# Optimization experiments

Hardware: AMD Instinct MI355X
Metric: run time of the kernel (lower is better)

The kernel has to match this reference:

```python
import jax, jax.numpy as jnp
import numpy as np

B, T_PREFIX, C_IN = 8, 6144, 8
OUT_LEN, OUT_C = 2048, 8
AUX_DIM = 16
D_MODEL, D_STATE, HEADDIM, EXPAND = 256, 32, 64, 2
D_INNER = EXPAND * D_MODEL            # 512
NHEADS = D_INNER // HEADDIM           # 8
CONV_DIM = D_INNER + 2 * D_STATE      # 576
D_PROJ = 2 * D_INNER + 2 * D_STATE + NHEADS  # 1096
N_LAYERS = 2
CHUNK = 64
PATCH = 16
PRECONV_K = 5
DCONV_K = 4


def setup_inputs() -> dict:
    key = jax.random.key(0)
    ks = iter(jax.random.split(key, 64))
    def rn(shape, s=0.02):
        return s * jax.random.normal(next(ks), shape, jnp.float32)
    inp = dict(
        x_prefix=jax.random.normal(next(ks), (B, T_PREFIX, C_IN), jnp.float32),
        y_aux=jax.random.normal(next(ks), (B, AUX_DIM), jnp.float32),
        pre_conv_w=rn((D_MODEL, C_IN, PRECONV_K), 0.1),
        pre_conv_b=rn((D_MODEL,)),
        patch_w=rn((D_MODEL, D_MODEL, PATCH), 0.05),
        patch_b=rn((D_MODEL,)),
        mask_token=rn((D_MODEL,)),
        aux_w=rn((AUX_DIM, D_MODEL), 0.1),
        aux_b=rn((D_MODEL,)),
        patch_out_w=rn((2 * D_MODEL, OUT_C * PATCH), 0.05),
        patch_out_b=rn((OUT_C * PATCH,)),
    )
    for d in ('fwd', 'bwd'):
        inp[f'{d}_norm_w'] = jnp.ones((N_LAYERS, D_MODEL), jnp.float32)
        inp[f'{d}_inproj'] = rn((N_LAYERS, D_MODEL, D_PROJ), 0.05)
        inp[f'{d}_conv_w'] = rn((N_LAYERS, CONV_DIM, DCONV_K), 0.2)
        inp[f'{d}_conv_b'] = rn((N_LAYERS, CONV_DIM))
        inp[f'{d}_dtbias'] = rn((N_LAYERS, NHEADS), 0.5)
        inp[f'{d}_Alog'] = jnp.tile(jnp.log(jnp.arange(1, NHEADS + 1, dtype=jnp.float32)), (N_LAYERS, 1))
        inp[f'{d}_D'] = jnp.ones((N_LAYERS, NHEADS), jnp.float32)
        inp[f'{d}_gnorm'] = jnp.ones((N_LAYERS, D_INNER), jnp.float32)
        inp[f'{d}_outproj'] = rn((N_LAYERS, D_INNER, D_MODEL), 0.05)
    return inp


def rmsnorm(x, w, eps=1e-5):
    return x * jax.lax.rsqrt(jnp.mean(x * x, axis=-1, keepdims=True) + eps) * w


def conv1d(x, w, b, stride, pad):  # x: [B,C,T], w: [O,I,K]
    y = jax.lax.conv_general_dilated(x, w, (stride,), [(pad, pad)],
                                     dimension_numbers=('NCH', 'OIH', 'NCH'))
    return y + b[None, :, None]


def mamba_block(u, inproj, conv_w, conv_b, dtbias, Alog, Dp, gnorm_w, outproj):
    # Mamba-2/SSD style block: in_proj -> z | xBC | dt, causal depthwise conv,
    # selective scan with per-head scalar decay A, +D skip, gated RMSNorm, out_proj.
    b, T, _ = u.shape
    zxbcdt = u @ inproj                                   # [b,T,D_PROJ]
    z = zxbcdt[..., :D_INNER]
    xBC = zxbcdt[..., D_INNER:D_INNER + CONV_DIM]
    dt = jax.nn.softplus(zxbcdt[..., -NHEADS:] + dtbias)  # [b,T,H]
    # causal depthwise conv over time
    xc = jax.lax.conv_general_dilated(xBC.transpose(0, 2, 1), conv_w[:, None, :], (1,),
                                      [(DCONV_K - 1, 0)],
                                      dimension_numbers=('NCH', 'OIH', 'NCH'),
                                      feature_group_count=CONV_DIM)
    xBC = jax.nn.silu((xc + conv_b[None, :, None]).transpose(0, 2, 1))
    xs = xBC[..., :D_INNER].reshape(b, T, NHEADS, HEADDIM)  # [b,T,H,P]
    Bm = xBC[..., D_INNER:D_INNER + D_STATE]                # [b,T,N]
    Cm = xBC[..., D_INNER + D_STATE:]                       # [b,T,N]
    A = -jnp.exp(Alog)                                      # [H]

    def step(h, inps):  # h: [b,H,P,N]
        dt_t, x_t, B_t, C_t = inps
        dA = jnp.exp(dt_t * A)[:, :, None, None]
        h = h * dA + (dt_t[:, :, None] * x_t)[..., None] * B_t[:, None, None, :]
        y = jnp.einsum('bhpn,bn->bhp', h, C_t)
        return h, y

    h0 = jnp.zeros((b, NHEADS, HEADDIM, D_STATE), u.dtype)
    _, ys = jax.lax.scan(step, h0, (dt.transpose(1, 0, 2), xs.transpose(1, 0, 2, 3),
                                    Bm.transpose(1, 0, 2), Cm.transpose(1, 0, 2)))
    y = ys.transpose(1, 0, 2, 3) + Dp[None, None, :, None] * xs
    y = y.reshape(b, T, D_INNER)
    y = rmsnorm(y * jax.nn.silu(z), gnorm_w)
    return y @ outproj


def reference(x_prefix, y_aux, pre_conv_w, pre_conv_b, patch_w, patch_b, mask_token,
              aux_w, aux_b, fwd_norm_w, fwd_inproj, fwd_conv_w, fwd_conv_b, fwd_dtbias,
              fwd_Alog, fwd_D, fwd_gnorm, fwd_outproj, bwd_norm_w, bwd_inproj,
              bwd_conv_w, bwd_conv_b, bwd_dtbias, bwd_Alog, bwd_D, bwd_gnorm,
              bwd_outproj, patch_out_w, patch_out_b):
    b = x_prefix.shape[0]
    t_total = T_PREFIX + OUT_LEN
    x_full = jnp.pad(x_prefix, ((0, 0), (0, OUT_LEN), (0, 0)))        # zeros for future
    x = jax.nn.silu(conv1d(x_full.transpose(0, 2, 1), pre_conv_w, pre_conv_b, 1, PRECONV_K // 2))
    x = conv1d(x, patch_w, patch_b, PATCH, 0).transpose(0, 2, 1)      # [b, n_tokens, d_model]
    n_tokens = x.shape[1]
    # eval mode: deterministic future-patch mask, dropout is identity
    starts = jnp.arange(n_tokens) * PATCH
    mask = (starts >= T_PREFIX)[None, :, None]
    x = jnp.where(mask, mask_token[None, None, :], x)
    aux_bias = jax.nn.silu(y_aux @ aux_w + aux_b)[:, None, :]
    x = x + aux_bias
    pad_t = (-n_tokens) % CHUNK
    if pad_t:
        x = jnp.pad(x, ((0, 0), (0, pad_t), (0, 0)))
    h_f = x
    h_b = x[:, ::-1]
    for i in range(N_LAYERS):
        h_f = h_f + mamba_block(rmsnorm(h_f, fwd_norm_w[i]), fwd_inproj[i], fwd_conv_w[i],
                                fwd_conv_b[i], fwd_dtbias[i], fwd_Alog[i], fwd_D[i],
                                fwd_gnorm[i], fwd_outproj[i])
        h_b = h_b + mamba_block(rmsnorm(h_b, bwd_norm_w[i]), bwd_inproj[i], bwd_conv_w[i],
                                bwd_conv_b[i], bwd_dtbias[i], bwd_Alog[i], bwd_D[i],
                                bwd_gnorm[i], bwd_outproj[i])
    h = jnp.concatenate([h_f, h_b[:, ::-1]], axis=-1)[:, :n_tokens]   # [b,n,2*d_model]
    patch_pred = h @ patch_out_w + patch_out_b                        # [b,n,out_c*patch]
    y = patch_pred.reshape(b, n_tokens, OUT_C, PATCH).reshape(b, n_tokens * PATCH, OUT_C)
    y = y[:, :t_total, :]
    return y[:, T_PREFIX:, :]
```

## Files before the change

kernel.cpp:

```cpp
#include <hip/hip_runtime.h>
#include <hip/hip_bf16.h>
#include <math.h>

#define BSZ      8
#define TPREF    6144
#define CIN      8
#define DMODEL   256
#define DINNER   512
#define DSTATE   32
#define NHEADS   8
#define HEADDIM  64
#define CONVDIM  576
#define DPROJ    1096
#define NTOK     512
#define NVIS     384
#define TBWD     128
#define MFWD     (BSZ * NTOK)
#define MBWD     (BSZ * TBWD)
#define MALL     (MFWD + MBWD)

typedef float f32x4 __attribute__((ext_vector_type(4)));
typedef __bf16 bf16x8 __attribute__((ext_vector_type(8)));

__device__ __forceinline__ float silu_f(float x) { return x / (1.f + expf(-x)); }

#define ASYNC16(gp, lp) \
    __builtin_amdgcn_global_load_lds((const __attribute__((address_space(1))) void*)(gp), \
                                     (__attribute__((address_space(3))) void*)(lp), 16, 0, 0)

__global__ __launch_bounds__(256) void gemm_mfma(
    const __bf16* __restrict__ A, const __bf16* __restrict__ Bt,
    float* __restrict__ C, const float* __restrict__ bias,
    int N, int K, int ldc, int flags, long pstr) {
    __shared__ char sm[16384];
    int tid = threadIdx.x;
    int m0 = blockIdx.y * 128, n0 = blockIdx.x * 128;
    int klen = K / gridDim.z;
    int kbeg = blockIdx.z * klen;
    int w = tid >> 6, l = tid & 63;
    int wm = w >> 1, wn = w & 1;
    int lm = l & 15, q = l >> 4;

    f32x4 acc[4][4];
    #pragma unroll
    for (int i = 0; i < 4; i++)
        #pragma unroll
        for (int j = 0; j < 4; j++) acc[i][j] = (f32x4)0.f;

    for (int k0 = 0; k0 < klen; k0 += 32) {
        int kb = kbeg + k0;
        #pragma unroll
        for (int i = 0; i < 2; i++) {
            int s = i * 256 + tid;
            ASYNC16(A + (size_t)(m0 + (s >> 2)) * K + kb + (s & 3) * 8, sm + s * 16);
        }
        #pragma unroll
        for (int i = 0; i < 2; i++) {
            int s = i * 256 + tid;
            ASYNC16(Bt + (size_t)(n0 + (s >> 2)) * K + kb + (s & 3) * 8, sm + 8192 + s * 16);
        }
        __syncthreads();
        bf16x8 af[4], bfr[4];
        #pragma unroll
        for (int mf = 0; mf < 4; mf++)
            af[mf] = *(const bf16x8*)(sm + (wm * 64 + mf * 16 + lm) * 64 + q * 16);
        #pragma unroll
        for (int nf = 0; nf < 4; nf++)
            bfr[nf] = *(const bf16x8*)(sm + 8192 + (wn * 64 + nf * 16 + lm) * 64 + q * 16);
        #pragma unroll
        for (int mf = 0; mf < 4; mf++)
            #pragma unroll
            for (int nf = 0; nf < 4; nf++)
                acc[mf][nf] = __builtin_amdgcn_mfma_f32_16x16x32_bf16(af[mf], bfr[nf], acc[mf][nf], 0, 0, 0);
        __syncthreads();
    }

    #pragma unroll
    for (int mf = 0; mf < 4; mf++) {
        int mbase = m0 + wm * 64 + mf * 16 + q * 4;
        #pragma unroll
        for (int nf = 0; nf < 4; nf++) {
            int n = n0 + wn * 64 + nf * 16 + lm;
            if (n < N) {
                #pragma unroll
                for (int r = 0; r < 4; r++) {
                    float v = acc[mf][nf][r];
                    size_t ci = (size_t)(mbase + r) * ldc + n;
                    if (flags & 4) {
                        v = silu_f(v + bias[n]);
                        ((__bf16*)C)[ci] = (__bf16)v;
                    } else if (flags & 8) {
                        C[ci + (size_t)blockIdx.z * pstr] = v;
                    } else if (flags & 2) {
                        atomicAdd(C + ci, v);
                    } else {
                        C[ci] = v;
                    }
                }
            }
        }
    }
}

__global__ __launch_bounds__(256) void gemm_inproj(
    const __bf16* __restrict__ u, const __bf16* __restrict__ ipTf,
    const __bf16* __restrict__ ipTb, float* __restrict__ C) {
    __shared__ char sm[16384];
    int tid = threadIdx.x;
    int m0 = blockIdx.y * 128, n0 = blockIdx.x * 128;
    const __bf16* Bt = (m0 >= MFWD) ? ipTb : ipTf;
    int w = tid >> 6, l = tid & 63;
    int wm = w >> 1, wn = w & 1, lm = l & 15, q = l >> 4;
    f32x4 acc[4][4];
    #pragma unroll
    for (int i = 0; i < 4; i++)
        #pragma unroll
        for (int j = 0; j < 4; j++) acc[i][j] = (f32x4)0.f;
    for (int k0 = 0; k0 < 256; k0 += 32) {
        #pragma unroll
        for (int i = 0; i < 2; i++) {
            int s = i * 256 + tid;
            ASYNC16(u + (size_t)(m0 + (s >> 2)) * 256 + k0 + (s & 3) * 8, sm + s * 16);
        }
        #pragma unroll
        for (int i = 0; i < 2; i++) {
            int s = i * 256 + tid;
            ASYNC16(Bt + (size_t)(n0 + (s >> 2)) * 256 + k0 + (s & 3) * 8, sm + 8192 + s * 16);
        }
        __syncthreads();
        bf16x8 af[4], bfr[4];
        #pragma unroll
        for (int mf = 0; mf < 4; mf++)
            af[mf] = *(const bf16x8*)(sm + (wm * 64 + mf * 16 + lm) * 64 + q * 16);
        #pragma unroll
        for (int nf = 0; nf < 4; nf++)
            bfr[nf] = *(const bf16x8*)(sm + 8192 + (wn * 64 + nf * 16 + lm) * 64 + q * 16);
        #pragma unroll
        for (int mf = 0; mf < 4; mf++)
            #pragma unroll
            for (int nf = 0; nf < 4; nf++)
                acc[mf][nf] = __builtin_amdgcn_mfma_f32_16x16x32_bf16(af[mf], bfr[nf], acc[mf][nf], 0, 0, 0);
        __syncthreads();
    }
    #pragma unroll
    for (int mf = 0; mf < 4; mf++) {
        int mbase = m0 + wm * 64 + mf * 16 + q * 4;
        #pragma unroll
        for (int nf = 0; nf < 4; nf++) {
            int n = n0 + wn * 64 + nf * 16 + lm;
            if (n < DPROJ) {
                #pragma unroll
                for (int r = 0; r < 4; r++)
                    C[(size_t)(mbase + r) * DPROJ + n] = acc[mf][nf][r];
            }
        }
    }
}

__global__ __launch_bounds__(256) void gemm_outproj(
    const __bf16* __restrict__ y2, const __bf16* __restrict__ opTf,
    const __bf16* __restrict__ opTb, float* __restrict__ C, int layer) {
    __shared__ char sm[16384];
    int tid = threadIdx.x;
    int yb = blockIdx.y;
    int m0 = (layer == 0) ? yb * 128
                          : ((yb < 8) ? (yb * 512 + 384) : (MFWD + (yb - 8) * 128));
    int n0 = blockIdx.x * 128;
    const __bf16* Bt = (m0 >= MFWD) ? opTb : opTf;
    int w = tid >> 6, l = tid & 63;
    int wm = w >> 1, wn = w & 1, lm = l & 15, q = l >> 4;
    f32x4 acc[4][4];
    #pragma unroll
    for (int i = 0; i < 4; i++)
        #pragma unroll
        for (int j = 0; j < 4; j++) acc[i][j] = (f32x4)0.f;
    for (int k0 = 0; k0 < 512; k0 += 32) {
        #pragma unroll
        for (int i = 0; i < 2; i++) {
            int s = i * 256 + tid;
            ASYNC16(y2 + (size_t)(m0 + (s >> 2)) * 512 + k0 + (s & 3) * 8, sm + s * 16);
        }
        #pragma unroll
        for (int i = 0; i < 2; i++) {
            int s = i * 256 + tid;
            ASYNC16(Bt + (size_t)(n0 + (s >> 2)) * 512 + k0 + (s & 3) * 8, sm + 8192 + s * 16);
        }
        __syncthreads();
        bf16x8 af[4], bfr[4];
        #pragma unroll
        for (int mf = 0; mf < 4; mf++)
            af[mf] = *(const bf16x8*)(sm + (wm * 64 + mf * 16 + lm) * 64 + q * 16);
        #pragma unroll
        for (int nf = 0; nf < 4; nf++)
            bfr[nf] = *(const bf16x8*)(sm + 8192 + (wn * 64 + nf * 16 + lm) * 64 + q * 16);
        #pragma unroll
        for (int mf = 0; mf < 4; mf++)
            #pragma unroll
            for (int nf = 0; nf < 4; nf++)
                acc[mf][nf] = __builtin_amdgcn_mfma_f32_16x16x32_bf16(af[mf], bfr[nf], acc[mf][nf], 0, 0, 0);
        __syncthreads();
    }
    #pragma unroll
    for (int mf = 0; mf < 4; mf++) {
        int mbase = m0 + wm * 64 + mf * 16 + q * 4;
        #pragma unroll
        for (int nf = 0; nf < 4; nf++) {
            int n = n0 + wn * 64 + nf * 16 + lm;
            #pragma unroll
            for (int r = 0; r < 4; r++) {
                size_t ci = (size_t)(mbase + r) * DMODEL + n;
                C[ci] += acc[mf][nf][r];
            }
        }
    }
}

__global__ __launch_bounds__(256) void rmsnorm_all(
    const float* __restrict__ h, const float* __restrict__ wf,
    const float* __restrict__ wb, __bf16* __restrict__ u) {
    int row = blockIdx.x * 4 + (threadIdx.x >> 6);
    int lane = threadIdx.x & 63;
    const float* w = (row >= MFWD) ? wb : wf;
    float4 v = ((const float4*)(h + (size_t)row * 256))[lane];
    float ss = v.x * v.x + v.y * v.y + v.z * v.z + v.w * v.w;
    #pragma unroll
    for (int off = 32; off >= 1; off >>= 1) ss += __shfl_xor(ss, off);
    float rs = rsqrtf(ss * (1.f / 256.f) + 1e-5f);
    float4 wv = ((const float4*)w)[lane];
    __bf16 o4[4] = {(__bf16)(v.x * rs * wv.x), (__bf16)(v.y * rs * wv.y),
                    (__bf16)(v.z * rs * wv.z), (__bf16)(v.w * rs * wv.w)};
    *(uint2*)(u + (size_t)row * 256 + lane * 4) = *(uint2*)o4;
}

__global__ __launch_bounds__(256) void gatednorm_all(
    const __bf16* __restrict__ ysD, const float* __restrict__ zx,
    const float* __restrict__ gwf, const float* __restrict__ gwb,
    __bf16* __restrict__ y2) {
    int row = blockIdx.x * 4 + (threadIdx.x >> 6);
    int lane = threadIdx.x & 63;
    const float* gw = (row >= MFWD) ? gwb : gwf;
    union { uint4 u; __bf16 hh[8]; } yv;
    yv.u = *(const uint4*)(ysD + (size_t)row * 512 + lane * 8);
    const float4* zr = (const float4*)(zx + (size_t)row * DPROJ + lane * 8);
    float4 z0 = zr[0], z1 = zr[1];
    float g[8];
    g[0] = (float)yv.hh[0] * silu_f(z0.x); g[1] = (float)yv.hh[1] * silu_f(z0.y);
    g[2] = (float)yv.hh[2] * silu_f(z0.z); g[3] = (float)yv.hh[3] * silu_f(z0.w);
    g[4] = (float)yv.hh[4] * silu_f(z1.x); g[5] = (float)yv.hh[5] * silu_f(z1.y);
    g[6] = (float)yv.hh[6] * silu_f(z1.z); g[7] = (float)yv.hh[7] * silu_f(z1.w);
    float ss = 0.f;
    #pragma unroll
    for (int j = 0; j < 8; j++) ss += g[j] * g[j];
    #pragma unroll
    for (int off = 32; off >= 1; off >>= 1) ss += __shfl_xor(ss, off);
    float rs = rsqrtf(ss * (1.f / 512.f) + 1e-5f);
    const float4* gr = (const float4*)(gw + lane * 8);
    float4 g0 = gr[0], g1 = gr[1];
    union { uint4 u; __bf16 hh[8]; } d;
    d.hh[0] = (__bf16)(g[0] * rs * g0.x); d.hh[1] = (__bf16)(g[1] * rs * g0.y);
    d.hh[2] = (__bf16)(g[2] * rs * g0.z); d.hh[3] = (__bf16)(g[3] * rs * g0.w);
    d.hh[4] = (__bf16)(g[4] * rs * g1.x); d.hh[5] = (__bf16)(g[5] * rs * g1.y);
    d.hh[6] = (__bf16)(g[6] * rs * g1.z); d.hh[7] = (__bf16)(g[7] * rs * g1.w);
    *(uint4*)(y2 + (size_t)row * 512 + lane * 8) = d.u;
}

__global__ void prep_all(const float* __restrict__ pre_conv_w, const float* __restrict__ patch_w,
                         const float* __restrict__ ip0, const float* __restrict__ ip1,
                         const float* __restrict__ op0, const float* __restrict__ op1,
                         const float* __restrict__ pow_, const float* __restrict__ pob,
                         const float* __restrict__ y_aux, const float* __restrict__ aux_w,
                         const float* __restrict__ aux_b, const float* __restrict__ xp,
                         __bf16* __restrict__ WpreT, __bf16* __restrict__ WtT,
                         __bf16* __restrict__ inprojT, __bf16* __restrict__ outprojT,
                         __bf16* __restrict__ poT, float* __restrict__ auxb,
                         float* __restrict__ dout, __bf16* __restrict__ Aim) {
    __shared__ float tile[32][33];
    int bx = blockIdx.x, tid = threadIdx.x;
    int tx = tid & 31, ty = tid >> 5;
    if (bx < 256) {
        int o = bx, c = tid;
        float f[16];
        const float4* s = (const float4*)(patch_w + (size_t)o * 4096 + c * 16);
        #pragma unroll
        for (int j = 0; j < 4; j++) *(float4*)&f[j * 4] = s[j];
        #pragma unroll
        for (int k = 0; k < 16; k++)
            WtT[(size_t)o * 4096 + k * 256 + c] = (__bf16)f[k];
        return;
    }
    bx -= 256;
    if (bx < 1152) {
        int seg = bx / 288, rem = bx % 288;
        int n0 = (rem / 8) * 32, k0 = (rem % 8) * 32;
        const float* src = (seg < 2 ? ip0 : ip1) + (size_t)(seg & 1) * 256 * DPROJ;
        #pragma unroll
        for (int j = 0; j < 4; j++) {
            int r = ty + j * 8;
            int n = n0 + tx;
            tile[r][tx] = (n < DPROJ) ? src[(size_t)(k0 + r) * DPROJ + n] : 0.f;
        }
        __syncthreads();
        __bf16* dst = inprojT + (size_t)seg * 1152 * 256;
        #pragma unroll
        for (int j = 0; j < 4; j++) {
            int r = ty + j * 8;
            dst[(size_t)(n0 + r) * 256 + k0 + tx] = (__bf16)tile[tx][r];
        }
        return;
    }
    bx -= 1152;
    if (bx < 512) {
        int s = bx / 128, rem = bx % 128;
        int n0 = (rem / 16) * 32, k0 = (rem % 16) * 32;
        const float* src = (s < 2 ? op0 : op1) + (size_t)(s & 1) * DINNER * DMODEL;
        #pragma unroll
        for (int j = 0; j < 4; j++) {
            int r = ty + j * 8;
            tile[r][tx] = src[(size_t)(k0 + r) * 256 + n0 + tx];
        }
        __syncthreads();
        __bf16* dst = outprojT + (size_t)s * 256 * 512;
        #pragma unroll
        for (int j = 0; j < 4; j++) {
            int r = ty + j * 8;
            dst[(size_t)(n0 + r) * 512 + k0 + tx] = (__bf16)tile[tx][r];
        }
        return;
    }
    bx -= 512;
    if (bx < 64) {
        int n0 = (bx / 16) * 32, k0 = (bx % 16) * 32;
        #pragma unroll
        for (int j = 0; j < 4; j++) {
            int r = ty + j * 8;
            tile[r][tx] = pow_[(size_t)(k0 + r) * 128 + n0 + tx];
        }
        __syncthreads();
        #pragma unroll
        for (int j = 0; j < 4; j++) {
            int r = ty + j * 8;
            poT[(size_t)(n0 + r) * 512 + k0 + tx] = (__bf16)tile[tx][r];
        }
        return;
    }
    bx -= 64;
    if (bx < 64) {
        int idx = bx * 256 + tid;
        int o = idx >> 6, kk = idx & 63;
        WpreT[idx] = (kk < 40) ? (__bf16)pre_conv_w[o * 40 + kk] : (__bf16)0.f;
        return;
    }
    bx -= 64;
    if (bx < 512) {
        int idx = bx * 256 + tid;
        dout[idx] = pob[idx & 127];
        return;
    }
    bx -= 512;
    if (bx < 192) {
        int m = bx * 256 + tid;
        int t = m % TPREF, b = m / TPREF;
        __bf16 d[64];
        #pragma unroll
        for (int k = 0; k < 5; k++) {
            int tt = t - 2 + k;
            bool ok = (tt >= 0) && (tt < TPREF);
            const float* s = xp + ((size_t)b * TPREF + tt) * 8;
            #pragma unroll
            for (int i = 0; i < 8; i++)
                d[i * 5 + k] = ok ? (__bf16)s[i] : (__bf16)0.f;
        }
        #pragma unroll
        for (int j = 40; j < 64; j++) d[j] = (__bf16)0.f;
        uint4* o = (uint4*)(Aim + (size_t)m * 64);
        #pragma unroll
        for (int k = 0; k < 8; k++) o[k] = ((const uint4*)d)[k];
        return;
    }
    bx -= 192;
    {
        int b = bx, o = tid;
        float acc = aux_b[o];
        #pragma unroll
        for (int i = 0; i < 16; i++) acc += y_aux[b * 16 + i] * aux_w[i * 256 + o];
        auxb[b * 256 + o] = silu_f(acc);
    }
}

__global__ void assemble_kernel(const float* __restrict__ Cp4, const float* __restrict__ pb,
                                const float* __restrict__ mtok, const float* __restrict__ aux,
                                float* __restrict__ h_all) {
    int idx = blockIdx.x * 256 + threadIdx.x;
    if (idx >= BSZ * NTOK * DMODEL) return;
    int o = idx & 255, tok = (idx >> 8) & 511, b = idx >> 17;
    float v;
    if (tok < NVIS) {
        size_t ci = (size_t)(b * NVIS + tok) * 256 + o;
        v = pb[o] + Cp4[ci] + Cp4[ci + (size_t)3072 * 256] +
            Cp4[ci + (size_t)2 * 3072 * 256] + Cp4[ci + (size_t)3 * 3072 * 256];
    } else {
        v = mtok[o];
    }
    v += aux[b * 256 + o];
    h_all[idx] = v;
    if (tok >= NVIS)
        h_all[(size_t)MFWD * 256 + (size_t)(b * TBWD + (NTOK - 1 - tok)) * 256 + o] = v;
}

__global__ __launch_bounds__(256) void dwconv2_kernel(
    const float* __restrict__ zx, const float* __restrict__ cwf, const float* __restrict__ cbf,
    const float* __restrict__ cwb, const float* __restrict__ cbb,
    __bf16* __restrict__ XtF, __bf16* __restrict__ XtB,
    __bf16* __restrict__ BCF, __bf16* __restrict__ BCB) {
    int cg = blockIdx.x;
    int id = blockIdx.y;
    int b, t0, T; size_t rowbase;
    const float *cw, *cb; __bf16 *Xt, *BC;
    if (id < 64) { b = id >> 3; t0 = (id & 7) * 64; T = NTOK; rowbase = (size_t)b * NTOK;
                   cw = cwf; cb = cbf; Xt = XtF; BC = BCF; }
    else { int i2 = id - 64; b = i2 >> 1; t0 = (i2 & 1) * 64; T = TBWD;
           rowbase = (size_t)MFWD + (size_t)b * TBWD; cw = cwb; cb = cbb; Xt = XtB; BC = BCB; }
    int c0 = cg * 64;
    __shared__ float xs[67][65];
    int lane = threadIdx.x & 63, grp = threadIdx.x >> 6;
    for (int r = grp; r < 67; r += 4) {
        int t = t0 - 3 + r;
        xs[r][lane] = (t >= 0) ? zx[(rowbase + t) * DPROJ + DINNER + c0 + lane] : 0.f;
    }
    __syncthreads();
    if (cg < 8) {
        int t = lane;
        #pragma unroll
        for (int ci = grp; ci < 64; ci += 4) {
            int c = c0 + ci;
            float acc = cb[c];
            #pragma unroll
            for (int k = 0; k < 4; k++) acc += cw[c * 4 + k] * xs[t + k][ci];
            Xt[((size_t)((b * 8 + cg) * 64 + ci)) * T + t0 + t] = (__bf16)silu_f(acc);
        }
    } else {
        int c = lane;
        #pragma unroll
        for (int ti = grp; ti < 64; ti += 4) {
            float acc = cb[c0 + c];
            #pragma unroll
            for (int k = 0; k < 4; k++) acc += cw[(c0 + c) * 4 + k] * xs[ti + k][c];
            BC[((size_t)(b * T + t0 + ti)) * 64 + c] = (__bf16)silu_f(acc);
        }
    }
}

__global__ __launch_bounds__(64) void scan_local(
    const __bf16* __restrict__ XtF, const __bf16* __restrict__ XtB,
    const __bf16* __restrict__ BCF, const __bf16* __restrict__ BCB,
    const float* __restrict__ zx,
    const float* __restrict__ dtbf, const float* __restrict__ dtbb,
    const float* __restrict__ Alogf, const float* __restrict__ Alogb,
    const float* __restrict__ Dpf, const float* __restrict__ Dpb,
    __bf16* __restrict__ ysD,
    __bf16* __restrict__ ChatF, __bf16* __restrict__ ChatB,
    float* __restrict__ dSF, float* __restrict__ dSB,
    float* __restrict__ DcsF, float* __restrict__ DcsB, int layer) {
    int id = blockIdx.x, hd = blockIdx.y;
    int b, c, T, NC; size_t rowbase;
    const __bf16 *Xt, *BC; __bf16* Chat; float *dS, *Dcs;
    const float *dtb, *Alog, *Dp;
    if (id < 64) { b = id >> 3; c = id & 7; T = NTOK; NC = 8; rowbase = (size_t)b * NTOK;
                   Xt = XtF; BC = BCF; Chat = ChatF; dS = dSF; Dcs = DcsF;
                   dtb = dtbf; Alog = Alogf; Dp = Dpf; }
    else { int i2 = id - 64; b = i2 >> 1; c = i2 & 1; T = TBWD; NC = 2;
           rowbase = (size_t)MFWD + (size_t)b * TBWD;
           Xt = XtB; BC = BCB; Chat = ChatB; dS = dSB; Dcs = DcsB;
           dtb = dtbb; Alog = Alogb; Dp = Dpb; }
    bool skipY = (layer == 1) && (id < 64) && (c < 6);
    int bh = b * 8 + hd;
    int t0 = c * 64;
    int lane = threadIdx.x;
    int lm = lane & 15, q = lane >> 4;
    float A = -expf(Alog[hd]);
    float Dh = Dp[hd];

    __shared__ char smem[23552];
    __bf16 (*Xl)[72]  = (__bf16(*)[72])(smem);
    __bf16 (*BCl)[72] = (__bf16(*)[72])(smem + 9216);
    __bf16 (*Pl)[72]  = (__bf16(*)[72])(smem + 9216);
    __bf16 (*Wbl)[72] = (__bf16(*)[72])(smem + 18432);
    float* lcs = (float*)(smem + 23040);
    float* dts = (float*)(smem + 23296);

    const uint4* xg = (const uint4*)(Xt + (size_t)(bh * 64 + lane) * T + t0);
    const uint4* bg = (const uint4*)(BC + ((size_t)(b * T + t0 + lane)) * 64);
    uint4 xv[8], bv[8];
    #pragma unroll
    for (int k = 0; k < 8; k++) { xv[k] = xg[k]; bv[k] = bg[k]; }
    float xdt = zx[(rowbase + t0 + lane) * DPROJ + 1088 + hd] + dtb[hd];
    float dtv = (xdt > 20.f) ? xdt : log1pf(expf(xdt));
    #pragma unroll
    for (int k = 0; k < 8; k++) {
        *(uint4*)&Xl[lane][k * 8] = xv[k];
        if (!skipY) *(uint4*)&BCl[lane][k * 8] = bv[k];
    }
    float lc = A * dtv;
    #pragma unroll
    for (int off = 1; off < 64; off <<= 1) {
        float o = __shfl_up(lc, off);
        if (lane >= off) lc += o;
    }
    lcs[lane] = lc; dts[lane] = dtv;
    float lc63 = __shfl(lc, 63);
    float wj = expf(lc63 - lc) * dtv;
    float eli = expf(lc);
    float Dc = expf(lc63);
    if (lane == 0) Dcs[bh * NC + c] = Dc;
    if (!skipY) {
        __bf16* co = Chat + ((size_t)(bh * NC + c) * 64 + lane) * 32;
        #pragma unroll
        for (int k = 0; k < 4; k++) {
            union { uint4 u; __bf16 h[8]; } s; s.u = bv[4 + k];
            union { uint4 u; __bf16 h[8]; } d;
            #pragma unroll
            for (int j = 0; j < 8; j++) d.h[j] = (__bf16)(eli * (float)s.h[j]);
            *(uint4*)(co + k * 8) = d.u;
        }
    }
    #pragma unroll
    for (int k = 0; k < 4; k++) {
        union { uint4 u; __bf16 h[8]; } s; s.u = bv[k];
        #pragma unroll
        for (int j = 0; j < 8; j++) Wbl[k * 8 + j][lane] = (__bf16)(wj * (float)s.h[j]);
    }
    __syncthreads();

    bf16x8 xf0[4], xf1[4];
    if (!skipY) {
        bf16x8 cfr[4], bfr[4];
        #pragma unroll
        for (int t4 = 0; t4 < 4; t4++) {
            cfr[t4] = *(const bf16x8*)&BCl[t4 * 16 + lm][32 + q * 8];
            bfr[t4] = *(const bf16x8*)&BCl[t4 * 16 + lm][q * 8];
        }
        #pragma unroll
        for (int ti = 0; ti < 4; ti++) {
            float lci[4];
            #pragma unroll
            for (int r = 0; r < 4; r++) lci[r] = lcs[ti * 16 + q * 4 + r];
            #pragma unroll
            for (int tj = 0; tj < 4; tj++) {
                if (tj > ti) {
                    #pragma unroll
                    for (int r = 0; r < 4; r++) Pl[ti * 16 + q * 4 + r][tj * 16 + lm] = (__bf16)0.f;
                    continue;
                }
                f32x4 g = __builtin_amdgcn_mfma_f32_16x16x32_bf16(cfr[ti], bfr[tj], (f32x4)0.f, 0, 0, 0);
                int j = tj * 16 + lm;
                float lcj = lcs[j], dtj = dts[j];
                #pragma unroll
                for (int r = 0; r < 4; r++) {
                    int i = ti * 16 + q * 4 + r;
                    float v = (j <= i) ? g[r] * expf(lci[r] - lcj) * dtj : 0.f;
                    if (j == i) v += Dh;
                    Pl[i][j] = (__bf16)v;
                }
            }
        }
        __syncthreads();

        bf16x8 pf0[4], pf1[4];
        #pragma unroll
        for (int t4 = 0; t4 < 4; t4++) {
            pf0[t4] = *(const bf16x8*)&Pl[t4 * 16 + lm][q * 8];
            pf1[t4] = *(const bf16x8*)&Pl[t4 * 16 + lm][32 + q * 8];
            xf0[t4] = *(const bf16x8*)&Xl[t4 * 16 + lm][q * 8];
            xf1[t4] = *(const bf16x8*)&Xl[t4 * 16 + lm][32 + q * 8];
        }
        #pragma unroll
        for (int ti = 0; ti < 4; ti++) {
            #pragma unroll
            for (int tp = 0; tp < 4; tp++) {
                f32x4 y = __builtin_amdgcn_mfma_f32_16x16x32_bf16(pf0[ti], xf0[tp], (f32x4)0.f, 0, 0, 0);
                y = __builtin_amdgcn_mfma_f32_16x16x32_bf16(pf1[ti], xf1[tp], y, 0, 0, 0);
                #pragma unroll
                for (int r = 0; r < 4; r++) {
                    int i = ti * 16 + q * 4 + r;
                    ysD[(rowbase + t0 + i) * DINNER + hd * 64 + tp * 16 + lm] = (__bf16)y[r];
                }
            }
        }
    } else {
        #pragma unroll
        for (int t4 = 0; t4 < 4; t4++) {
            xf0[t4] = *(const bf16x8*)&Xl[t4 * 16 + lm][q * 8];
            xf1[t4] = *(const bf16x8*)&Xl[t4 * 16 + lm][32 + q * 8];
        }
    }
    bf16x8 wf0[2], wf1[2];
    #pragma unroll
    for (int tn = 0; tn < 2; tn++) {
        wf0[tn] = *(const bf16x8*)&Wbl[tn * 16 + lm][q * 8];
        wf1[tn] = *(const bf16x8*)&Wbl[tn * 16 + lm][32 + q * 8];
    }
    float* dso = dS + (size_t)(bh * NC + c) * 2048;
    #pragma unroll
    for (int tp = 0; tp < 4; tp++) {
        #pragma unroll
        for (int tn = 0; tn < 2; tn++) {
            f32x4 s = __builtin_amdgcn_mfma_f32_16x16x32_bf16(xf0[tp], wf0[tn], (f32x4)0.f, 0, 0, 0);
            s = __builtin_amdgcn_mfma_f32_16x16x32_bf16(xf1[tp], wf1[tn], s, 0, 0, 0);
            #pragma unroll
            for (int r = 0; r < 4; r++) {
                int pp = tp * 16 + q * 4 + r, nn = tn * 16 + lm;
                dso[pp * 32 + nn] = s[r];
            }
        }
    }
}

__global__ __launch_bounds__(256) void scan_tail(
    const float* __restrict__ dSF, const float* __restrict__ dSB,
    const float* __restrict__ DcsF, const float* __restrict__ DcsB,
    const __bf16* __restrict__ ChatF, const __bf16* __restrict__ ChatB,
    __bf16* __restrict__ ysD, int layer) {
    int blk = blockIdx.x;
    int dir = blk >= 64;
    int bh = blk & 63;
    int NC = dir ? 2 : 8;
    int T = dir ? TBWD : NTOK;
    int b = bh >> 3, hd = bh & 7;
    size_t rowbase = dir ? ((size_t)MFWD + (size_t)b * TBWD) : ((size_t)b * NTOK);
    const float* dS = dir ? dSB : dSF;
    const float* Dcs = dir ? DcsB : DcsF;
    const __bf16* Chat = dir ? ChatB : ChatF;
    int cmin = (layer == 1 && !dir) ? 6 : 1;
    int tid = threadIdx.x;
    __shared__ __bf16 Spl[8][64][40];
    {
        int p = tid >> 2, n0 = (tid & 3) * 8;
        float S[8];
        #pragma unroll
        for (int j = 0; j < 8; j++) S[j] = 0.f;
        for (int c = 0; c < NC; c++) {
            union { uint4 u; __bf16 hh[8]; } o;
            #pragma unroll
            for (int j = 0; j < 8; j++) o.hh[j] = (__bf16)S[j];
            *(uint4*)&Spl[c][p][n0] = o.u;
            float Dc = Dcs[bh * NC + c];
            const float4* dp = (const float4*)(dS + ((size_t)(bh * NC + c)) * 2048 + tid * 8);
            float4 d0 = dp[0], d1 = dp[1];
            S[0] = Dc * S[0] + d0.x; S[1] = Dc * S[1] + d0.y;
            S[2] = Dc * S[2] + d0.z; S[3] = Dc * S[3] + d0.w;
            S[4] = Dc * S[4] + d1.x; S[5] = Dc * S[5] + d1.y;
            S[6] = Dc * S[6] + d1.z; S[7] = Dc * S[7] + d1.w;
        }
    }
    __syncthreads();
    int w = tid >> 6, l = tid & 63, lm = l & 15, q = l >> 4;
    for (int c = cmin + w; c < NC; c += 4) {
        int t0 = c * 64;
        const __bf16* Cb = Chat + (size_t)(bh * NC + c) * 2048;
        bf16x8 cf[4], sf[4];
        #pragma unroll
        for (int t4 = 0; t4 < 4; t4++) {
            cf[t4] = *(const bf16x8*)(Cb + (t4 * 16 + lm) * 32 + q * 8);
            sf[t4] = *(const bf16x8*)&Spl[c][t4 * 16 + lm][q * 8];
        }
        #pragma unroll
        for (int ti = 0; ti < 4; ti++) {
            #pragma unroll
            for (int tp = 0; tp < 4; tp++) {
                f32x4 y = __builtin_amdgcn_mfma_f32_16x16x32_bf16(cf[ti], sf[tp], (f32x4)0.f, 0, 0, 0);
                #pragma unroll
                for (int r = 0; r < 4; r++) {
                    int i = ti * 16 + q * 4 + r;
                    size_t idx = (rowbase + t0 + i) * DINNER + hd * 64 + tp * 16 + lm;
                    ysD[idx] = (__bf16)((float)ysD[idx] + y[r]);
                }
            }
        }
    }
}

__global__ void hcat_kernel(const float* __restrict__ h_all, __bf16* __restrict__ hc) {
    int idx = blockIdx.x * 256 + threadIdx.x;
    if (idx >= BSZ * TBWD * DINNER) return;
    int c = idx & 511, j = (idx >> 9) & 127, b = idx >> 16;
    float v = (c < 256) ? h_all[(size_t)(b * NTOK + NVIS + j) * 256 + c]
                        : h_all[(size_t)MFWD * 256 + (size_t)(b * TBWD + (TBWD - 1 - j)) * 256 + (c - 256)];
    hc[idx] = (__bf16)v;
}

extern "C" void kernel_launch(void* const* d_in, const int* in_sizes, int n_in,
                              void* d_out, int out_size, void* d_ws, size_t ws_size,
                              hipStream_t stream) {
    const float* x_prefix    = (const float*)d_in[0];
    const float* y_aux       = (const float*)d_in[1];
    const float* pre_conv_w  = (const float*)d_in[2];
    const float* pre_conv_b  = (const float*)d_in[3];
    const float* patch_w     = (const float*)d_in[4];
    const float* patch_b     = (const float*)d_in[5];
    const float* mask_token  = (const float*)d_in[6];
    const float* aux_w       = (const float*)d_in[7];
    const float* aux_b       = (const float*)d_in[8];
    const float* patch_out_w = (const float*)d_in[9];
    const float* patch_out_b = (const float*)d_in[10];
    const float* w_norm[2]   = {(const float*)d_in[11], (const float*)d_in[20]};
    const float* w_inproj[2] = {(const float*)d_in[12], (const float*)d_in[21]};
    const float* w_convw[2]  = {(const float*)d_in[13], (const float*)d_in[22]};
    const float* w_convb[2]  = {(const float*)d_in[14], (const float*)d_in[23]};
    const float* w_dtb[2]    = {(const float*)d_in[15], (const float*)d_in[24]};
    const float* w_alog[2]   = {(const float*)d_in[16], (const float*)d_in[25]};
    const float* w_D[2]      = {(const float*)d_in[17], (const float*)d_in[26]};
    const float* w_gnorm[2]  = {(const float*)d_in[18], (const float*)d_in[27]};
    const float* w_outproj[2]= {(const float*)d_in[19], (const float*)d_in[28]};

    char* p = (char*)d_ws;
    auto alloc = [&](size_t bytes) { char* r = p; p += (bytes + 255) & ~255ULL; return r; };
    __bf16* A_patch  = (__bf16*)alloc((size_t)3072 * 4096 * 2);
    __bf16* Aim      = (__bf16*)alloc((size_t)BSZ * TPREF * 64 * 2);
    __bf16* WpreT    = (__bf16*)alloc((size_t)256 * 64 * 2);
    __bf16* WtT      = (__bf16*)alloc((size_t)256 * 4096 * 2);
    __bf16* inprojT  = (__bf16*)alloc((size_t)4 * 1152 * 256 * 2);
    __bf16* outprojT = (__bf16*)alloc((size_t)4 * 256 * 512 * 2);
    __bf16* poT      = (__bf16*)alloc((size_t)128 * 512 * 2);
    float*  auxb     = (float*)alloc(8 * 256 * 4);
    float*  Cp4      = (float*)alloc((size_t)4 * 3072 * 256 * 4);
    float*  h_all    = (float*)alloc((size_t)MALL * 256 * 4);
    __bf16* u        = (__bf16*)alloc((size_t)MALL * 256 * 2);
    float*  zx       = (float*)alloc((size_t)MALL * DPROJ * 4);
    __bf16* XtF      = (__bf16*)alloc((size_t)64 * 64 * NTOK * 2);
    __bf16* XtB      = (__bf16*)alloc((size_t)64 * 64 * TBWD * 2);
    __bf16* BCF      = (__bf16*)alloc((size_t)BSZ * NTOK * 64 * 2);
    __bf16* BCB      = (__bf16*)alloc((size_t)BSZ * TBWD * 64 * 2);
    __bf16* ysD      = (__bf16*)alloc((size_t)MALL * DINNER * 2);
    __bf16* y2       = (__bf16*)alloc((size_t)MALL * DINNER * 2);
    __bf16* hct      = (__bf16*)alloc((size_t)1024 * DINNER * 2);
    __bf16* ChatF    = (__bf16*)alloc((size_t)64 * 8 * 2048 * 2);
    __bf16* ChatB    = (__bf16*)alloc((size_t)64 * 2 * 2048 * 2);
    float*  dSF      = (float*)alloc((size_t)64 * 8 * 2048 * 4);
    float*  dSB      = (float*)alloc((size_t)64 * 2 * 2048 * 4);
    float*  DcsF     = (float*)alloc((size_t)64 * 8 * 4);
    float*  DcsB     = (float*)alloc((size_t)64 * 2 * 4);

    prep_all<<<256 + 1152 + 512 + 64 + 64 + 512 + 192 + 8, 256, 0, stream>>>(
        pre_conv_w, patch_w, w_inproj[0], w_inproj[1], w_outproj[0], w_outproj[1],
        patch_out_w, patch_out_b, y_aux, aux_w, aux_b, x_prefix,
        WpreT, WtT, inprojT, outprojT, poT, auxb, (float*)d_out, Aim);
    gemm_mfma<<<dim3(2, (BSZ * TPREF) / 128, 1), 256, 0, stream>>>(
        Aim, WpreT, (float*)A_patch, pre_conv_b, 256, 64, 256, 4, 0);
    gemm_mfma<<<dim3(2, 24, 4), 256, 0, stream>>>(
        A_patch, WtT, Cp4, nullptr, 256, 4096, 256, 8, (long)3072 * 256);
    assemble_kernel<<<(BSZ * NTOK * DMODEL) / 256, 256, 0, stream>>>(
        Cp4, patch_b, mask_token, auxb, h_all);

    for (int i = 0; i < 2; i++) {
        const __bf16* ipTf = inprojT + (size_t)(0 * 2 + i) * 1152 * 256;
        const __bf16* ipTb = inprojT + (size_t)(1 * 2 + i) * 1152 * 256;
        const __bf16* opTf = outprojT + (size_t)(0 * 2 + i) * 256 * 512;
        const __bf16* opTb = outprojT + (size_t)(1 * 2 + i) * 256 * 512;
        rmsnorm_all<<<MALL / 4, 256, 0, stream>>>(h_all, w_norm[0] + i * 256, w_norm[1] + i * 256, u);
        gemm_inproj<<<dim3(9, MALL / 128), 256, 0, stream>>>(u, ipTf, ipTb, zx);
        dwconv2_kernel<<<dim3(9, 80), 256, 0, stream>>>(
            zx, w_convw[0] + i * CONVDIM * 4, w_convb[0] + i * CONVDIM,
            w_convw[1] + i * CONVDIM * 4, w_convb[1] + i * CONVDIM,
            XtF, XtB, BCF, BCB);
        scan_local<<<dim3(80, NHEADS), 64, 0, stream>>>(
            XtF, XtB, BCF, BCB, zx,
            w_dtb[0] + i * 8, w_dtb[1] + i * 8,
            w_alog[0] + i * 8, w_alog[1] + i * 8,
            w_D[0] + i * 8, w_D[1] + i * 8,
            ysD, ChatF, ChatB, dSF, dSB, DcsF, DcsB, i);
        scan_tail<<<128, 256, 0, stream>>>(dSF, dSB, DcsF, DcsB, ChatF, ChatB, ysD, i);
        gatednorm_all<<<MALL / 4, 256, 0, stream>>>(
            ysD, zx, w_gnorm[0] + i * DINNER, w_gnorm[1] + i * DINNER, y2);
        int oy = (i == 0) ? (MALL / 128) : 16;
        gemm_outproj<<<dim3(2, oy), 256, 0, stream>>>(y2, opTf, opTb, h_all, i);
    }

    hcat_kernel<<<(BSZ * TBWD * DINNER) / 256, 256, 0, stream>>>(h_all, hct);
    gemm_mfma<<<dim3(1, 8, 4), 256, 0, stream>>>(
        hct, poT, (float*)d_out, nullptr, 128, 512, 128, 2, 0);
}
```

Baseline: 339.6 us.

## Fuse patch assembly into split-K atomics, store zx as bf16, fuse final concat

The patch GEMM now uses 8-way split-K and atomically accumulates directly into h_all. prep_all pre-initializes h_all with bias, mask token and aux bias, which removes the Cp4 partial buffer and the assemble kernel. The in-projection output is stored as bf16 for the z/xBC columns, with dt kept in a separate small fp32 array, to cut memory traffic for the conv, scan and gated-norm kernels. The final projection reads h_all directly and converts it to bf16 in LDS, which removes hcat_kernel. The costs are reduced precision on z/xBC, more atomic contention, and nondeterministic summation order.

Result: no change. 340.3 us, median of 2 (+0.2%).

```diff
diff --git a/kernel.cpp b/kernel.cpp
--- a/kernel.cpp
+++ b/kernel.cpp
@@ -12,6 +12,7 @@
 #define HEADDIM  64
 #define CONVDIM  576
 #define DPROJ    1096
+#define ZXW      1088
 #define NTOK     512
 #define NVIS     384
 #define TBWD     128
@@ -31,7 +32,7 @@
 __global__ __launch_bounds__(256) void gemm_mfma(
     const __bf16* __restrict__ A, const __bf16* __restrict__ Bt,
     float* __restrict__ C, const float* __restrict__ bias,
-    int N, int K, int ldc, int flags, long pstr) {
+    int N, int K, int ldc, int flags) {
     __shared__ char sm[16384];
     int tid = threadIdx.x;
     int m0 = blockIdx.y * 128, n0 = blockIdx.x * 128;
@@ -85,16 +86,17 @@
                 #pragma unroll
                 for (int r = 0; r < 4; r++) {
                     float v = acc[mf][nf][r];
-                    size_t ci = (size_t)(mbase + r) * ldc + n;
                     if (flags & 4) {
                         v = silu_f(v + bias[n]);
-                        ((__bf16*)C)[ci] = (__bf16)v;
-                    } else if (flags & 8) {
-                        C[ci + (size_t)blockIdx.z * pstr] = v;
+                        ((__bf16*)C)[(size_t)(mbase + r) * ldc + n] = (__bf16)v;
+                    } else if (flags & 16) {
+                        int mm = mbase + r;
+                        int bb = mm / NVIS, tk = mm - bb * NVIS;
+                        atomicAdd(C + ((size_t)(bb * NTOK + tk)) * 256 + n, v);
                     } else if (flags & 2) {
-                        atomicAdd(C + ci, v);
+                        atomicAdd(C + (size_t)(mbase + r) * ldc + n, v);
                     } else {
-                        C[ci] = v;
+                        C[(size_t)(mbase + r) * ldc + n] = v;
                     }
                 }
             }
@@ -102,9 +104,75 @@
     }
 }
 
+__global__ __launch_bounds__(256) void final_gemm(
+    const float* __restrict__ h_all, const __bf16* __restrict__ poT,
+    float* __restrict__ out) {
+    __shared__ __bf16 Asm_[128][40];
+    __shared__ char Bsm[8192];
+    int tid = threadIdx.x;
+    int m0 = blockIdx.y * 128;
+    int z = blockIdx.z;
+    int w = tid >> 6, l = tid & 63;
+    int wm = w >> 1, wn_ = w & 1, lm = l & 15, q = l >> 4;
+    f32x4 acc[4][4];
+    #pragma unroll
+    for (int i = 0; i < 4; i++)
+        #pragma unroll
+        for (int j = 0; j < 4; j++) acc[i][j] = (f32x4)0.f;
+
+    int r = tid >> 1, half = tid & 1;
+    int m = m0 + r;
+    int b = m >> 7, jj = m & 127;
+    size_t arow = (z == 0) ? ((size_t)(b * NTOK + NVIS + jj) * 256)
+                           : ((size_t)MFWD * 256 + (size_t)(b * TBWD + (TBWD - 1 - jj)) * 256);
+    for (int k0 = 0; k0 < 256; k0 += 32) {
+        {
+            const float4* sp = (const float4*)(h_all + arow + k0 + half * 16);
+            float4 v0 = sp[0], v1 = sp[1], v2 = sp[2], v3 = sp[3];
+            union { uint4 u; __bf16 hh[8]; } d0, d1;
+            d0.hh[0] = (__bf16)v0.x; d0.hh[1] = (__bf16)v0.y; d0.hh[2] = (__bf16)v0.z; d0.hh[3] = (__bf16)v0.w;
+            d0.hh[4] = (__bf16)v1.x; d0.hh[5] = (__bf16)v1.y; d0.hh[6] = (__bf16)v1.z; d0.hh[7] = (__bf16)v1.w;
+            d1.hh[0] = (__bf16)v2.x; d1.hh[1] = (__bf16)v2.y; d1.hh[2] = (__bf16)v2.z; d1.hh[3] = (__bf16)v2.w;
+            d1.hh[4] = (__bf16)v3.x; d1.hh[5] = (__bf16)v3.y; d1.hh[6] = (__bf16)v3.z; d1.hh[7] = (__bf16)v3.w;
+            *(uint4*)&Asm_[r][half * 16] = d0.u;
+            *(uint4*)&Asm_[r][half * 16 + 8] = d1.u;
+        }
+        #pragma unroll
+        for (int i = 0; i < 2; i++) {
+            int s = i * 256 + tid;
+            ASYNC16(poT + (size_t)(s >> 2) * 512 + z * 256 + k0 + (s & 3) * 8, Bsm + s * 16);
+        }
+        __syncthreads();
+        bf16x8 af[4], bfr[4];
+        #pragma unroll
+        for (int mf = 0; mf < 4; mf++)
+            af[mf] = *(const bf16x8*)&Asm_[wm * 64 + mf * 16 + lm][q * 8];
+        #pragma unroll
+        for (int nf = 0; nf < 4; nf++)
+            bfr[nf] = *(const bf16x8*)(Bsm + (wn_ * 64 + nf * 16 + lm) * 64 + q * 16);
+        #pragma unroll
+        for (int mf = 0; mf < 4; mf++)
+            #pragma unroll
+            for (int nf = 0; nf < 4; nf++)
+                acc[mf][nf] = __builtin_amdgcn_mfma_f32_16x16x32_bf16(af[mf], bfr[nf], acc[mf][nf], 0, 0, 0);
+        __syncthreads();
+    }
+    #pragma unroll
+    for (int mf = 0; mf < 4; mf++) {
+        int mbase = m0 + wm * 64 + mf * 16 + q * 4;
+        #pragma unroll
+        for (int nf = 0; nf < 4; nf++) {
+            int n = wn_ * 64 + nf * 16 + lm;
+            #pragma unroll
+            for (int rr = 0; rr < 4; rr++)
+                atomicAdd(out + (size_t)(mbase + rr) * 128 + n, acc[mf][nf][rr]);
+        }
+    }
+}
+
 __global__ __launch_bounds__(256) void gemm_inproj(
     const __bf16* __restrict__ u, const __bf16* __restrict__ ipTf,
-    const __bf16* __restrict__ ipTb, float* __restrict__ C) {
+    const __bf16* __restrict__ ipTb, __bf16* __restrict__ zxb, float* __restrict__ dtc) {
     __shared__ char sm[16384];
     int tid = threadIdx.x;
     int m0 = blockIdx.y * 128, n0 = blockIdx.x * 128;
@@ -148,10 +216,11 @@
         #pragma unroll
         for (int nf = 0; nf < 4; nf++) {
             int n = n0 + wn * 64 + nf * 16 + lm;
-            if (n < DPROJ) {
-                #pragma unroll
-                for (int r = 0; r < 4; r++)
-                    C[(size_t)(mbase + r) * DPROJ + n] = acc[mf][nf][r];
+            #pragma unroll
+            for (int r = 0; r < 4; r++) {
+                float v = acc[mf][nf][r];
+                if (n < ZXW) zxb[(size_t)(mbase + r) * ZXW + n] = (__bf16)v;
+                else if (n < DPROJ) dtc[(size_t)(mbase + r) * 8 + (n - ZXW)] = v;
             }
         }
     }
@@ -233,21 +302,18 @@
 }
 
 __global__ __launch_bounds__(256) void gatednorm_all(
-    const __bf16* __restrict__ ysD, const float* __restrict__ zx,
+    const __bf16* __restrict__ ysD, const __bf16* __restrict__ zxb,
     const float* __restrict__ gwf, const float* __restrict__ gwb,
     __bf16* __restrict__ y2) {
     int row = blockIdx.x * 4 + (threadIdx.x >> 6);
     int lane = threadIdx.x & 63;
     const float* gw = (row >= MFWD) ? gwb : gwf;
-    union { uint4 u; __bf16 hh[8]; } yv;
+    union { uint4 u; __bf16 hh[8]; } yv, zv;
     yv.u = *(const uint4*)(ysD + (size_t)row * 512 + lane * 8);
-    const float4* zr = (const float4*)(zx + (size_t)row * DPROJ + lane * 8);
-    float4 z0 = zr[0], z1 = zr[1];
+    zv.u = *(const uint4*)(zxb + (size_t)row * ZXW + lane * 8);
     float g[8];
-    g[0] = (float)yv.hh[0] * silu_f(z0.x); g[1] = (float)yv.hh[1] * silu_f(z0.y);
-    g[2] = (float)yv.hh[2] * silu_f(z0.z); g[3] = (float)yv.hh[3] * silu_f(z0.w);
-    g[4] = (float)yv.hh[4] * silu_f(z1.x); g[5] = (float)yv.hh[5] * silu_f(z1.y);
-    g[6] = (float)yv.hh[6] * silu_f(z1.z); g[7] = (float)yv.hh[7] * silu_f(z1.w);
+    #pragma unroll
+    for (int j = 0; j < 8; j++) g[j] = (float)yv.hh[j] * silu_f((float)zv.hh[j]);
     float ss = 0.f;
     #pragma unroll
     for (int j = 0; j < 8; j++) ss += g[j] * g[j];
@@ -270,10 +336,11 @@
                          const float* __restrict__ pow_, const float* __restrict__ pob,
                          const float* __restrict__ y_aux, const float* __restrict__ aux_w,
                          const float* __restrict__ aux_b, const float* __restrict__ xp,
+                         const float* __restrict__ patch_b, const float* __restrict__ mtok,
                          __bf16* __restrict__ WpreT, __bf16* __restrict__ WtT,
                          __bf16* __restrict__ inprojT, __bf16* __restrict__ outprojT,
-                         __bf16* __restrict__ poT, float* __restrict__ auxb,
-                         float* __restrict__ dout, __bf16* __restrict__ Aim) {
+                         __bf16* __restrict__ poT, float* __restrict__ dout,
+                         __bf16* __restrict__ Aim, float* __restrict__ h_all) {
     __shared__ float tile[32][33];
     int bx = blockIdx.x, tid = threadIdx.x;
     int tx = tid & 31, ty = tid >> 5;
@@ -379,36 +446,20 @@
     }
     bx -= 192;
     {
-        int b = bx, o = tid;
+        int row = bx, o = tid;
+        int b; bool masked;
+        if (row < MFWD) { b = row >> 9; int tok = row & 511; masked = (tok >= NVIS); }
+        else { b = (row - MFWD) >> 7; masked = true; }
         float acc = aux_b[o];
         #pragma unroll
         for (int i = 0; i < 16; i++) acc += y_aux[b * 16 + i] * aux_w[i * 256 + o];
-        auxb[b * 256 + o] = silu_f(acc);
-    }
-}
-
-__global__ void assemble_kernel(const float* __restrict__ Cp4, const float* __restrict__ pb,
-                                const float* __restrict__ mtok, const float* __restrict__ aux,
-                                float* __restrict__ h_all) {
-    int idx = blockIdx.x * 256 + threadIdx.x;
-    if (idx >= BSZ * NTOK * DMODEL) return;
-    int o = idx & 255, tok = (idx >> 8) & 511, b = idx >> 17;
-    float v;
-    if (tok < NVIS) {
-        size_t ci = (size_t)(b * NVIS + tok) * 256 + o;
-        v = pb[o] + Cp4[ci] + Cp4[ci + (size_t)3072 * 256] +
-            Cp4[ci + (size_t)2 * 3072 * 256] + Cp4[ci + (size_t)3 * 3072 * 256];
-    } else {
-        v = mtok[o];
-    }
-    v += aux[b * 256 + o];
-    h_all[idx] = v;
-    if (tok >= NVIS)
-        h_all[(size_t)MFWD * 256 + (size_t)(b * TBWD + (NTOK - 1 - tok)) * 256 + o] = v;
+        float v = (masked ? mtok[o] : patch_b[o]) + silu_f(acc);
+        h_all[(size_t)row * 256 + o] = v;
+    }
 }
 
 __global__ __launch_bounds__(256) void dwconv2_kernel(
-    const float* __restrict__ zx, const float* __restrict__ cwf, const float* __restrict__ cbf,
+    const __bf16* __restrict__ zxb, const float* __restrict__ cwf, const float* __restrict__ cbf,
     const float* __restrict__ cwb, const float* __restrict__ cbb,
     __bf16* __restrict__ XtF, __bf16* __restrict__ XtB,
     __bf16* __restrict__ BCF, __bf16* __restrict__ BCB) {
@@ -425,7 +476,7 @@
     int lane = threadIdx.x & 63, grp = threadIdx.x >> 6;
     for (int r = grp; r < 67; r += 4) {
         int t = t0 - 3 + r;
-        xs[r][lane] = (t >= 0) ? zx[(rowbase + t) * DPROJ + DINNER + c0 + lane] : 0.f;
+        xs[r][lane] = (t >= 0) ? (float)zxb[(rowbase + t) * ZXW + DINNER + c0 + lane] : 0.f;
     }
     __syncthreads();
     if (cg < 8) {
@@ -453,7 +504,7 @@
 __global__ __launch_bounds__(64) void scan_local(
     const __bf16* __restrict__ XtF, const __bf16* __restrict__ XtB,
     const __bf16* __restrict__ BCF, const __bf16* __restrict__ BCB,
-    const float* __restrict__ zx,
+    const float* __restrict__ dtc,
     const float* __restrict__ dtbf, const float* __restrict__ dtbb,
     const float* __restrict__ Alogf, const float* __restrict__ Alogb,
     const float* __restrict__ Dpf, const float* __restrict__ Dpb,
@@ -493,7 +544,7 @@
     uint4 xv[8], bv[8];
     #pragma unroll
     for (int k = 0; k < 8; k++) { xv[k] = xg[k]; bv[k] = bg[k]; }
-    float xdt = zx[(rowbase + t0 + lane) * DPROJ + 1088 + hd] + dtb[hd];
+    float xdt = dtc[(rowbase + t0 + lane) * 8 + hd] + dtb[hd];
     float dtv = (xdt > 20.f) ? xdt : log1pf(expf(xdt));
     #pragma unroll
     for (int k = 0; k < 8; k++) {
@@ -677,15 +728,6 @@
             }
         }
     }
-}
-
-__global__ void hcat_kernel(const float* __restrict__ h_all, __bf16* __restrict__ hc) {
-    int idx = blockIdx.x * 256 + threadIdx.x;
-    if (idx >= BSZ * TBWD * DINNER) return;
-    int c = idx & 511, j = (idx >> 9) & 127, b = idx >> 16;
-    float v = (c < 256) ? h_all[(size_t)(b * NTOK + NVIS + j) * 256 + c]
-                        : h_all[(size_t)MFWD * 256 + (size_t)(b * TBWD + (TBWD - 1 - j)) * 256 + (c - 256)];
-    hc[idx] = (__bf16)v;
 }
 
 extern "C" void kernel_launch(void* const* d_in, const int* in_sizes, int n_in,
@@ -721,18 +763,16 @@
     __bf16* inprojT  = (__bf16*)alloc((size_t)4 * 1152 * 256 * 2);
     __bf16* outprojT = (__bf16*)alloc((size_t)4 * 256 * 512 * 2);
     __bf16* poT      = (__bf16*)alloc((size_t)128 * 512 * 2);
-    float*  auxb     = (float*)alloc(8 * 256 * 4);
-    float*  Cp4      = (float*)alloc((size_t)4 * 3072 * 256 * 4);
     float*  h_all    = (float*)alloc((size_t)MALL * 256 * 4);
     __bf16* u        = (__bf16*)alloc((size_t)MALL * 256 * 2);
-    float*  zx       = (float*)alloc((size_t)MALL * DPROJ * 4);
+    __bf16* zxb      = (__bf16*)alloc((size_t)MALL * ZXW * 2);
+    float*  dtc      = (float*)alloc((size_t)MALL * 8 * 4);
     __bf16* XtF      = (__bf16*)alloc((size_t)64 * 64 * NTOK * 2);
     __bf16* XtB      = (__bf16*)alloc((size_t)64 * 64 * TBWD * 2);
     __bf16* BCF      = (__bf16*)alloc((size_t)BSZ * NTOK * 64 * 2);
     __bf16* BCB      = (__bf16*)alloc((size_t)BSZ * TBWD * 64 * 2);
     __bf16* ysD      = (__bf16*)alloc((size_t)MALL * DINNER * 2);
     __bf16* y2       = (__bf16*)alloc((size_t)MALL * DINNER * 2);
-    __bf16* hct      = (__bf16*)alloc((size_t)1024 * DINNER * 2);
     __bf16* ChatF    = (__bf16*)alloc((size_t)64 * 8 * 2048 * 2);
     __bf16* ChatB    = (__bf16*)alloc((size_t)64 * 2 * 2048 * 2);
     float*  dSF      = (float*)alloc((size_t)64 * 8 * 2048 * 4);
@@ -740,16 +780,14 @@
     float*  DcsF     = (float*)alloc((size_t)64 * 8 * 4);
     float*  DcsB     = (float*)alloc((size_t)64 * 2 * 4);
 
-    prep_all<<<256 + 1152 + 512 + 64 + 64 + 512 + 192 + 8, 256, 0, stream>>>(
+    prep_all<<<256 + 1152 + 512 + 64 + 64 + 512 + 192 + MALL, 256, 0, stream>>>(
         pre_conv_w, patch_w, w_inproj[0], w_inproj[1], w_outproj[0], w_outproj[1],
-        patch_out_w, patch_out_b, y_aux, aux_w, aux_b, x_prefix,
-        WpreT, WtT, inprojT, outprojT, poT, auxb, (float*)d_out, Aim);
+        patch_out_w, patch_out_b, y_aux, aux_w, aux_b, x_prefix, patch_b, mask_token,
+        WpreT, WtT, inprojT, outprojT, poT, (float*)d_out, Aim, h_all);
     gemm_mfma<<<dim3(2, (BSZ * TPREF) / 128, 1), 256, 0, stream>>>(
-        Aim, WpreT, (float*)A_patch, pre_conv_b, 256, 64, 256, 4, 0);
-    gemm_mfma<<<dim3(2, 24, 4), 256, 0, stream>>>(
-        A_patch, WtT, Cp4, nullptr, 256, 4096, 256, 8, (long)3072 * 256);
-    assemble_kernel<<<(BSZ * NTOK * DMODEL) / 256, 256, 0, stream>>>(
-        Cp4, patch_b, mask_token, auxb, h_all);
+        Aim, WpreT, (float*)A_patch, pre_conv_b, 256, 64, 256, 4);
+    gemm_mfma<<<dim3(2, 24, 8), 256, 0, stream>>>(
+        A_patch, WtT, h_all, nullptr, 256, 4096, 256, 16);
 
     for (int i = 0; i < 2; i++) {
         const __bf16* ipTf = inprojT + (size_t)(0 * 2 + i) * 1152 * 256;
@@ -757,25 +795,23 @@
         const __bf16* opTf = outprojT + (size_t)(0 * 2 + i) * 256 * 512;
         const __bf16* opTb = outprojT + (size_t)(1 * 2 + i) * 256 * 512;
         rmsnorm_all<<<MALL / 4, 256, 0, stream>>>(h_all, w_norm[0] + i * 256, w_norm[1] + i * 256, u);
-        gemm_inproj<<<dim3(9, MALL / 128), 256, 0, stream>>>(u, ipTf, ipTb, zx);
+        gemm_inproj<<<dim3(9, MALL / 128), 256, 0, stream>>>(u, ipTf, ipTb, zxb, dtc);
         dwconv2_kernel<<<dim3(9, 80), 256, 0, stream>>>(
-            zx, w_convw[0] + i * CONVDIM * 4, w_convb[0] + i * CONVDIM,
+            zxb, w_convw[0] + i * CONVDIM * 4, w_convb[0] + i * CONVDIM,
             w_convw[1] + i * CONVDIM * 4, w_convb[1] + i * CONVDIM,
             XtF, XtB, BCF, BCB);
         scan_local<<<dim3(80, NHEADS), 64, 0, stream>>>(
-            XtF, XtB, BCF, BCB, zx,
+            XtF, XtB, BCF, BCB, dtc,
             w_dtb[0] + i * 8, w_dtb[1] + i * 8,
             w_alog[0] + i * 8, w_alog[1] + i * 8,
             w_D[0] + i * 8, w_D[1] + i * 8,
             ysD, ChatF, ChatB, dSF, dSB, DcsF, DcsB, i);
         scan_tail<<<128, 256, 0, stream>>>(dSF, dSB, DcsF, DcsB, ChatF, ChatB, ysD, i);
         gatednorm_all<<<MALL / 4, 256, 0, stream>>>(
-            ysD, zx, w_gnorm[0] + i * DINNER, w_gnorm[1] + i * DINNER, y2);
+            ysD, zxb, w_gnorm[0] + i * DINNER, w_gnorm[1] + i * DINNER, y2);
         int oy = (i == 0) ? (MALL / 128) : 16;
         gemm_outproj<<<dim3(2, oy), 256, 0, stream>>>(y2, opTf, opTb, h_all, i);
     }
 
-    hcat_kernel<<<(BSZ * TBWD * DINNER) / 256, 256, 0, stream>>>(h_all, hct);
-    gemm_mfma<<<dim3(1, 8, 4), 256, 0, stream>>>(
-        hct, poT, (float*)d_out, nullptr, 128, 512, 128, 2, 0);
-}
+    final_gemm<<<dim3(1, 8, 2), 256, 0, stream>>>(h_all, poT, (float*)d_out);
+}
```
